# Kernel optimization log

Hardware: AMD Instinct MI355X
Metric: run time of the kernel (lower is better)

The kernel has to match this reference:

```python
import jax, jax.numpy as jnp
import numpy as np

EMBED_DIM = 512
NUM_HEADS = 8
GLOBAL_MIX = 0.5


def setup_inputs() -> dict:
    key = jax.random.key(0)
    ks = jax.random.split(key, 7)
    B, L, E = 8, 1024, EMBED_DIM
    s = 1.0 / np.sqrt(E)
    x = jax.random.normal(ks[0], (B, L, E), dtype=jnp.float32)
    mask = jax.random.randint(ks[1], (B, L), 0, 2) > 0  # True = valid token
    Wq = jax.random.normal(ks[2], (E, E), dtype=jnp.float32) * s
    Wk = jax.random.normal(ks[3], (E, E), dtype=jnp.float32) * s
    Wv = jax.random.normal(ks[4], (E, E), dtype=jnp.float32) * s
    Wo = jax.random.normal(ks[5], (E, E), dtype=jnp.float32) * s
    G = jax.random.normal(ks[6], (L, L), dtype=jnp.float32)
    return {"x": x, "mask": mask, "Wq": Wq, "Wk": Wk, "Wv": Wv, "Wo": Wo, "G": G}


def _tanh_mha(x, mask, Wq, Wk, Wv, Wo, G):
    B, L, E = x.shape
    H = NUM_HEADS
    D = E // H
    scale = 1.0 / np.sqrt(D)
    dt = x.dtype
    fmax = jnp.finfo(dt).max
    tiny = jnp.finfo(dt).tiny

    def split_heads(t):  # (B,L,E) -> (B,H,L,D)
        return t.reshape(B, L, H, D).transpose(0, 2, 1, 3)

    q = split_heads(x @ Wq.T)
    k = split_heads(x @ Wk.T)
    v = split_heads(x @ Wv.T)

    scores = jnp.tanh(jnp.einsum('bhqd,bhkd->bhqk', q, k) * scale)
    key_valid = mask[:, None, None, :]  # (B,1,1,L)
    scores = jnp.where(key_valid, scores, -jnp.inf)

    finite = jnp.isfinite(scores)
    finite_scores = jnp.where(finite, scores, -fmax)
    m = jnp.max(finite_scores, axis=(1, 2, 3), keepdims=True)  # per-sample amax over heads+q+k
    m = jnp.where(jnp.isfinite(m), m, jnp.zeros_like(m))
    exp_scores = jnp.where(finite, jnp.exp(scores - m), jnp.zeros_like(scores))

    mf = mask.astype(dt)
    exp_scores = exp_scores * mf[:, None, None, :] * mf[:, None, :, None]
    denom = jnp.maximum(exp_scores.sum(axis=(1, 2, 3), keepdims=True), tiny)
    weights = exp_scores / denom
    # dropout p=0 -> identity; renorm pass kept for faithfulness
    renorm = jnp.maximum(weights.sum(axis=(1, 2, 3), keepdims=True), tiny)
    weights = weights / renorm

    # learnable global attention: softmax rows, clamp, mask, normalize over (q,k)
    activated = jnp.maximum(jax.nn.softmax(G, axis=-1), 0.0)  # (L,L)
    gscores = activated[None] * mf[:, None, :] * mf[:, :, None]  # (B,L,L)
    gsums = jnp.maximum(gscores.sum(axis=(1, 2), keepdims=True), tiny)
    gnorm = (gscores / gsums)[:, None]  # (B,1,L,L)
    weights = (1.0 - GLOBAL_MIX) * weights + GLOBAL_MIX * gnorm

    attended = jnp.einsum('bhqk,bhkd->bhqd', weights, v)
    attended = attended * mf[:, None, :, None]
    attended = attended.transpose(0, 2, 1, 3).reshape(B, L, E)
    return attended @ Wo.T


def reference(x, mask, Wq, Wk, Wv, Wo, G):
    return _tanh_mha(x, mask, Wq, Wk, Wv, Wo, G)
```

## Files before the change

### kernel.cpp

```cpp
#include <hip/hip_runtime.h>
#include <math.h>

#define B_ 8
#define L_ 1024
#define E_ 512
#define H_ 8
#define D_ 64
#define QSZ (B_*H_*L_*D_)
#define BLE ((size_t)B_*L_*E_)
#define TINYF 1.175494350822287508e-38f
#define SWK(r) ((((r) ^ ((r) >> 3))) & 7)

typedef unsigned short u16;
typedef __attribute__((ext_vector_type(8))) short bfrag;
typedef __attribute__((ext_vector_type(4))) float ffrag;
typedef __attribute__((ext_vector_type(16))) float ffrag16;
typedef __attribute__((ext_vector_type(4))) short vshort4;

#if __has_builtin(__builtin_amdgcn_exp2f)
#define EXP2F(x) __builtin_amdgcn_exp2f(x)
#else
#define EXP2F(x) __expf((x) * 0.6931471805599453f)
#endif
#if __has_builtin(__builtin_amdgcn_rcpf)
#define RCPF(x) __builtin_amdgcn_rcpf(x)
#else
#define RCPF(x) (1.0f / (x))
#endif

__device__ __forceinline__ u16 f2b(float f) {
  unsigned u = __float_as_uint(f);
  u += 0x7fffu + ((u >> 16) & 1u);
  return (u16)(u >> 16);
}
__device__ __forceinline__ unsigned pk2(float a, float b) {
  unsigned ua = __float_as_uint(a); ua += 0x7fffu + ((ua >> 16) & 1u);
  unsigned ub = __float_as_uint(b); ub += 0x7fffu + ((ub >> 16) & 1u);
  return (ua >> 16) | (ub & 0xffff0000u);
}
__device__ __forceinline__ float blo(unsigned u) { return __uint_as_float(u << 16); }
__device__ __forceinline__ float bhi(unsigned u) { return __uint_as_float(u & 0xffff0000u); }

__device__ __forceinline__ bfrag cvt8v(const float* __restrict__ src) {
  float4 a = *(const float4*)src;
  float4 b = *(const float4*)(src + 4);
  bfrag r;
  r[0]=(short)f2b(a.x); r[1]=(short)f2b(a.y); r[2]=(short)f2b(a.z); r[3]=(short)f2b(a.w);
  r[4]=(short)f2b(b.x); r[5]=(short)f2b(b.y); r[6]=(short)f2b(b.z); r[7]=(short)f2b(b.w);
  return r;
}

__device__ __forceinline__ void gll16(const void* g, void* l) {
  __builtin_amdgcn_global_load_lds(
      (const __attribute__((address_space(1))) void*)g,
      (__attribute__((address_space(3))) void*)l, 16, 0, 0);
}

__global__ __launch_bounds__(256) void prep_softmax_k(
    const float* __restrict__ x, const float* __restrict__ Wq,
    const float* __restrict__ Wk, const float* __restrict__ Wv,
    const float* __restrict__ Wo, const float* __restrict__ G,
    const int* __restrict__ mask,
    u16* __restrict__ xb, u16* __restrict__ Wb, u16* __restrict__ actb,
    float* __restrict__ R) {
  const int bid = blockIdx.x, t = threadIdx.x;
  __shared__ float sred[8];
  __shared__ float rred[4][8];
  if (bid < 2048) {
    size_t c = (size_t)bid * 256 + t;
    *(bfrag*)&xb[c * 8] = cvt8v(x + c * 8);
    return;
  }
  if (bid < 2560) {
    const int c2 = bid - 2048;
    const float* src = (c2 < 128) ? Wq : (c2 < 256) ? Wk : (c2 < 384) ? Wv : Wo;
    const size_t base = (size_t)(c2 >> 7) * 262144;
    const size_t cc = (size_t)(c2 & 127) * 256 + t;
    *(bfrag*)&Wb[base + cc * 8] = cvt8v(src + cc * 8);
    return;
  }
  const int q = bid - 2560;
  const int w = t >> 6, lane = t & 63;
  float4 g4 = ((const float4*)(G + (size_t)q * 1024))[t];
  float m = fmaxf(fmaxf(g4.x, g4.y), fmaxf(g4.z, g4.w));
#pragma unroll
  for (int off = 32; off > 0; off >>= 1) m = fmaxf(m, __shfl_down(m, off));
  if (lane == 0) sred[w] = m;
  __syncthreads();
  m = fmaxf(fmaxf(sred[0], sred[1]), fmaxf(sred[2], sred[3]));
  float e0 = __expf(g4.x - m), e1 = __expf(g4.y - m);
  float e2 = __expf(g4.z - m), e3 = __expf(g4.w - m);
  float s = e0 + e1 + e2 + e3;
#pragma unroll
  for (int off = 32; off > 0; off >>= 1) s += __shfl_down(s, off);
  if (lane == 0) sred[4 + w] = s;
  __syncthreads();
  const float inv = 1.0f / (sred[4] + sred[5] + sred[6] + sred[7]);
  const unsigned p0 = pk2(e0 * inv, e1 * inv);
  const unsigned p1 = pk2(e2 * inv, e3 * inv);
  *(uint2*)&actb[(size_t)q * 1024 + t * 4] = make_uint2(p0, p1);
  const float r0 = blo(p0), r1 = bhi(p0);
  const float r2 = blo(p1), r3 = bhi(p1);
  float rd[8];
#pragma unroll
  for (int b = 0; b < 8; ++b) {
    const int* mkp = mask + b * 1024 + t * 4;
    rd[b] = (mkp[0] ? r0 : 0.f) + (mkp[1] ? r1 : 0.f) +
            (mkp[2] ? r2 : 0.f) + (mkp[3] ? r3 : 0.f);
#pragma unroll
    for (int off = 32; off > 0; off >>= 1) rd[b] += __shfl_down(rd[b], off);
  }
  if (lane == 0)
#pragma unroll
    for (int b = 0; b < 8; ++b) rred[w][b] = rd[b];
  __syncthreads();
  if (t < 8) R[q * 8 + t] = rred[0][t] + rred[1][t] + rred[2][t] + rred[3][t];
}

__global__ __launch_bounds__(256) void proj_k(
    const u16* __restrict__ xb, const u16* __restrict__ Wb,
    const int* __restrict__ mask, const float* __restrict__ R,
    float* __restrict__ sums,
    u16* __restrict__ Qb, u16* __restrict__ Kb, u16* __restrict__ Vtb) {
  const int m0 = blockIdx.x * 128;
  const int n0 = blockIdx.y * 128;
  __shared__ __align__(16) u16 As[128 * 64];
  __shared__ __align__(16) u16 Bs[128 * 64];
  __shared__ float rr[4][8];
  const int t = threadIdx.x, w = t >> 6, lane = t & 63;
  const int l15 = lane & 15, quad = lane >> 4;
  const int mq = (w >> 1) * 64, nq = (w & 1) * 64;

  if (blockIdx.x == 0 && blockIdx.y == 0) {
    float a8[8] = {0,0,0,0,0,0,0,0};
    for (int q = t; q < 1024; q += 256)
#pragma unroll
      for (int b = 0; b < 8; ++b)
        if (mask[b * 1024 + q]) a8[b] += R[q * 8 + b];
#pragma unroll
    for (int b = 0; b < 8; ++b) {
#pragma unroll
      for (int off = 32; off > 0; off >>= 1) a8[b] += __shfl_down(a8[b], off);
    }
    if (lane == 0)
#pragma unroll
      for (int b = 0; b < 8; ++b) rr[w][b] = a8[b];
    __syncthreads();
    if (t < 8) {
      sums[t] = 0.0f;
      sums[8 + t] = rr[0][t] + rr[1][t] + rr[2][t] + rr[3][t];
    }
  }

  const ffrag fz = {0.f, 0.f, 0.f, 0.f};
  ffrag acc[4][4];
#pragma unroll
  for (int i = 0; i < 4; ++i)
#pragma unroll
    for (int j = 0; j < 4; ++j) acc[i][j] = fz;

  for (int kk = 0; kk < 512; kk += 64) {
    __syncthreads();
#pragma unroll
    for (int j = 0; j < 4; ++j) {
      const int c = w * 256 + j * 64 + lane;
      const int row = c >> 3, ck = (c & 7) ^ (row & 7);
      gll16(xb + (size_t)(m0 + row) * 512 + kk + ck * 8,
            &As[(size_t)(w * 256 + j * 64) * 8]);
    }
#pragma unroll
    for (int j = 0; j < 4; ++j) {
      const int c = w * 256 + j * 64 + lane;
      const int row = c >> 3, ck = (c & 7) ^ (row & 7);
      gll16(Wb + (size_t)(n0 + row) * 512 + kk + ck * 8,
            &Bs[(size_t)(w * 256 + j * 64) * 8]);
    }
    __syncthreads();
#pragma unroll
    for (int s = 0; s < 2; ++s) {
      bfrag av[4], bv[4];
#pragma unroll
      for (int i = 0; i < 4; ++i) {
        const int ar = mq + i * 16 + l15;
        av[i] = *(const bfrag*)&As[ar * 64 + (((quad + 4 * s) ^ (ar & 7)) << 3)];
        const int br = nq + i * 16 + l15;
        bv[i] = *(const bfrag*)&Bs[br * 64 + (((quad + 4 * s) ^ (br & 7)) << 3)];
      }
#pragma unroll
      for (int i = 0; i < 4; ++i)
#pragma unroll
        for (int j = 0; j < 4; ++j)
          acc[i][j] = __builtin_amdgcn_mfma_f32_16x16x32_bf16(av[i], bv[j], acc[i][j], 0, 0, 0);
    }
  }
  const int z = n0 >> 9;
  const int c0 = n0 & 511;
#pragma unroll
  for (int i = 0; i < 4; ++i) {
    const int mbase = m0 + mq + i * 16 + quad * 4;
    const int b = mbase >> 10, l0 = mbase & 1023;
#pragma unroll
    for (int j = 0; j < 4; ++j) {
      const int nc = c0 + nq + j * 16 + l15;
      const int h = nc >> 6, d = nc & 63;
      if (z == 0) {
        u16* dst = Qb + ((size_t)(b * 8 + h) * 1024 + l0) * 64 + d;
#pragma unroll
        for (int r = 0; r < 4; ++r) dst[(size_t)r * 64] = f2b(acc[i][j][r]);
      } else if (z == 1) {
        u16* dst = Kb + ((size_t)(b * 8 + h) * 1024 + l0) * 64 + d;
#pragma unroll
        for (int r = 0; r < 4; ++r) dst[(size_t)r * 64] = f2b(acc[i][j][r]);
      } else {
        vshort4 vs;
#pragma unroll
        for (int r = 0; r < 4; ++r)
          vs[r] = (short)(mask[b * 1024 + l0 + r] ? f2b(acc[i][j][r]) : (u16)0);
        *(vshort4*)(Vtb + ((size_t)(b * 8 + h) * 64 + d) * 1024 + l0) = vs;
      }
    }
  }
}

__global__ __launch_bounds__(256) void attn_gv_k(
    const u16* __restrict__ Qb, const u16* __restrict__ Kb,
    const u16* __restrict__ Vtb, const u16* __restrict__ actb,
    const int* __restrict__ mask,
    u16* __restrict__ AEb, u16* __restrict__ AGb, float* __restrict__ denom) {
  __shared__ __align__(16) u16 POOL[13320];
  const int t = threadIdx.x, w = t >> 6, lane = t & 63;
  const int l15 = lane & 15, quad = lane >> 4;

  if (blockIdx.x < 512) {
    u16* As = POOL;
    u16* Bs = POOL + 4096;
    const int mt = blockIdx.x & 127, nt = blockIdx.x >> 7;
    const int m0 = mt * 64, n0 = nt * 128;
    const int b = mt >> 4;
    const int q0 = (mt & 15) * 64;
    const int mq = (w >> 1) * 32, nq = (w & 1) * 64;
    const ffrag fz = {0.f, 0.f, 0.f, 0.f};
    ffrag acc[2][4];
#pragma unroll
    for (int i = 0; i < 2; ++i)
#pragma unroll
      for (int j = 0; j < 4; ++j) acc[i][j] = fz;

    for (int kk = 0; kk < 1024; kk += 64) {
      __syncthreads();
#pragma unroll
      for (int j = 0; j < 2; ++j) {
        const int c = w * 128 + j * 64 + lane;
        const int row = c >> 3, ck = (c & 7) ^ (row & 7);
        gll16(actb + (size_t)(q0 + row) * 1024 + kk + ck * 8,
              &As[(size_t)(w * 128 + j * 64) * 8]);
      }
#pragma unroll
      for (int j = 0; j < 4; ++j) {
        const int c = w * 256 + j * 64 + lane;
        const int row = c >> 3, ck = (c & 7) ^ (row & 7);
        gll16(Vtb + (size_t)(b * 512 + n0 + row) * 1024 + kk + ck * 8,
              &Bs[(size_t)(w * 256 + j * 64) * 8]);
      }
      __syncthreads();
#pragma unroll
      for (int s = 0; s < 2; ++s) {
        bfrag av[2], bv[4];
#pragma unroll
        for (int i = 0; i < 2; ++i) {
          const int ar = mq + i * 16 + l15;
          av[i] = *(const bfrag*)&As[ar * 64 + (((quad + 4 * s) ^ (ar & 7)) << 3)];
        }
#pragma unroll
        for (int j = 0; j < 4; ++j) {
          const int br = nq + j * 16 + l15;
          bv[j] = *(const bfrag*)&Bs[br * 64 + (((quad + 4 * s) ^ (br & 7)) << 3)];
        }
#pragma unroll
        for (int i = 0; i < 2; ++i)
#pragma unroll
          for (int j = 0; j < 4; ++j)
            acc[i][j] = __builtin_amdgcn_mfma_f32_16x16x32_bf16(av[i], bv[j], acc[i][j], 0, 0, 0);
      }
    }
#pragma unroll
    for (int i = 0; i < 2; ++i) {
      const int mbase = m0 + mq + i * 16 + quad * 4;
#pragma unroll
      for (int j = 0; j < 4; ++j) {
        const int n = n0 + nq + j * 16 + l15;
#pragma unroll
        for (int r = 0; r < 4; ++r)
          AGb[(size_t)(mbase + r) * 512 + n] = f2b(acc[i][j][r]);
      }
    }
    return;
  }

  const int aid = blockIdx.x - 512;
  const int qt = aid & 15;
  const int bh = aid >> 4;
  const int b = bh >> 3, h = bh & 7;
  u16* Ks = POOL;
  u16* Vs = POOL + 4096;
  u16* Es = POOL + 8192;
  u16* Ms = POOL + 12288;
  float* red4 = (float*)(POOL + 13312);
  const int l31 = lane & 31, hi = lane >> 5;
  const int qsb = w >> 1, msb = w & 1;
  const int qpb = w & 1, dpb = w >> 1;

  const u16* Kg = Kb + (size_t)bh * 65536;
  const u16* Vg = Vtb + (size_t)bh * 65536;

  const u16* Qrow = Qb + ((size_t)bh * 1024 + qt * 64 + qsb * 32 + l31) * 64;
  bfrag qf[4];
#pragma unroll
  for (int ko = 0; ko < 4; ++ko) qf[ko] = *(const bfrag*)(Qrow + ko * 16 + hi * 8);

  {
    int4 mi = *(const int4*)(mask + b * 1024 + t * 4);
    vshort4 mv;
    mv[0] = mi.x ? (short)0x3F80 : (short)0; mv[1] = mi.y ? (short)0x3F80 : (short)0;
    mv[2] = mi.z ? (short)0x3F80 : (short)0; mv[3] = mi.w ? (short)0x3F80 : (short)0;
    *(vshort4*)&Ms[t * 4] = mv;
  }

  auto stageK = [&](int kt) {
#pragma unroll
    for (int j = 0; j < 2; ++j) {
      const int c = w * 128 + j * 64 + lane;
      const int row = c >> 3, ck = (c & 7) ^ SWK(row);
      gll16(Kg + (size_t)(kt * 64 + row) * 64 + ck * 8,
            &Ks[(size_t)(w * 128 + j * 64) * 8]);
    }
  };
  auto stageV = [&](int kt) {
#pragma unroll
    for (int j = 0; j < 2; ++j) {
      const int c = w * 128 + j * 64 + lane;
      const int row = c >> 3, ck = (c & 7) ^ SWK(row);
      gll16(Vg + (size_t)row * 1024 + kt * 64 + ck * 8,
            &Vs[(size_t)(w * 128 + j * 64) * 8]);
    }
  };

  stageK(0); stageV(0);
  __syncthreads();

  ffrag16 accE, dacc;
#pragma unroll
  for (int i = 0; i < 16; ++i) { accE[i] = 0.f; dacc[i] = 0.f; }

  for (int kt = 0; kt < 16; ++kt) {
    ffrag16 st;
#pragma unroll
    for (int i = 0; i < 16; ++i) st[i] = 0.f;
    const int krow = msb * 32 + l31;
    const int kk7 = SWK(krow);
#pragma unroll
    for (int ko = 0; ko < 4; ++ko) {
      bfrag ak = *(const bfrag*)&Ks[krow * 64 + (((ko * 2 + hi) ^ kk7) << 3)];
      st = __builtin_amdgcn_mfma_f32_32x32x16_bf16(ak, qf[ko], st, 0, 0, 0);
    }
    const int qrow = qsb * 32 + l31;
    const int qk7 = SWK(qrow);
#pragma unroll
    for (int g = 0; g < 4; ++g) {
      float ee[4];
#pragma unroll
      for (int r = 0; r < 4; ++r) {
        const float tt = EXP2F(st[4 * g + r] * 0.360673760222f);
        ee[r] = EXP2F(RCPF(tt + 1.0f) * -2.88539008178f);
      }
      const int k0 = msb * 32 + g * 8 + hi * 4;
      *(uint2*)&Es[qrow * 64 + (((k0 >> 3) ^ qk7) << 3) + (k0 & 7)] =
          make_uint2(pk2(ee[0], ee[1]), pk2(ee[2], ee[3]));
    }
    __syncthreads();
    if (kt < 15) stageK(kt + 1);

    const int erow = qpb * 32 + l31;
    const int ek7 = SWK(erow);
    const int vrow = dpb * 32 + l31;
    const int vk7 = SWK(vrow);
#pragma unroll
    for (int ko = 0; ko < 4; ++ko) {
      const int co = ko * 2 + hi;
      bfrag ea = *(const bfrag*)&Es[erow * 64 + ((co ^ ek7) << 3)];
      bfrag bv = *(const bfrag*)&Vs[vrow * 64 + ((co ^ vk7) << 3)];
      accE = __builtin_amdgcn_mfma_f32_32x32x16_bf16(ea, bv, accE, 0, 0, 0);
      if (dpb == 0) {
        bfrag bm = *(const bfrag*)&Ms[kt * 64 + ko * 16 + hi * 8];
        dacc = __builtin_amdgcn_mfma_f32_32x32x16_bf16(ea, bm, dacc, 0, 0, 0);
      }
    }
    __syncthreads();
    if (kt < 15) stageV(kt + 1);
  }

  const size_t obase = ((size_t)(b * 1024 + qt * 64 + qpb * 32)) * 512
                       + h * 64 + dpb * 32 + l31;
#pragma unroll
  for (int r = 0; r < 16; ++r) {
    const int qloc = (r & 3) + 8 * (r >> 2) + 4 * hi;
    AEb[obase + (size_t)qloc * 512] = f2b(accE[r]);
  }
  float dsumv = 0.0f;
  if (l31 == 0 && dpb == 0) {
    const int qb0 = b * 1024 + qt * 64 + qpb * 32 + 4 * hi;
#pragma unroll
    for (int r = 0; r < 16; ++r) {
      const int q = qb0 + (r & 3) + 8 * (r >> 2);
      dsumv += mask[q] ? dacc[r] : 0.0f;
    }
    red4[qpb * 2 + hi] = dsumv;
  }
  __syncthreads();
  if (t == 0) atomicAdd(denom + b, red4[0] + red4[1] + red4[2] + red4[3]);
}

__global__ __launch_bounds__(256) void o_proj_k(
    const u16* __restrict__ AEb, const u16* __restrict__ AGb,
    const int* __restrict__ mask, const float* __restrict__ sums,
    const u16* __restrict__ Wb, float* __restrict__ out) {
  const int m0 = blockIdx.x * 128;
  const int n0 = blockIdx.y * 128;
  const int b = m0 >> 10;
  const float c1 = 0.5f / fmaxf(sums[b], TINYF);
  const float c2 = 0.5f / fmaxf(sums[8 + b], TINYF);
  __shared__ __align__(16) u16 As[128 * 64];
  __shared__ __align__(16) u16 Bs[128 * 64];
  const int t = threadIdx.x, w = t >> 6, lane = t & 63;
  const int l15 = lane & 15, quad = lane >> 4;
  const int mq = (w >> 1) * 64, nq = (w & 1) * 64;
  int rowi[4]; float c1r[4], c2r[4];
#pragma unroll
  for (int i = 0; i < 4; ++i) {
    const int c = t + i * 256;
    rowi[i] = c >> 3;
    const int mqv = mask[b * 1024 + ((m0 + rowi[i]) & 1023)];
    c1r[i] = mqv ? c1 : 0.0f;
    c2r[i] = mqv ? c2 : 0.0f;
  }
  const ffrag fz = {0.f, 0.f, 0.f, 0.f};
  ffrag acc[4][4];
#pragma unroll
  for (int i = 0; i < 4; ++i)
#pragma unroll
    for (int j = 0; j < 4; ++j) acc[i][j] = fz;

  for (int kk = 0; kk < 512; kk += 64) {
    __syncthreads();
#pragma unroll
    for (int i = 0; i < 4; ++i) {
      const int c = t + i * 256;
      const int row = rowi[i], ck = c & 7;
      const size_t gofs = (size_t)(m0 + row) * 512 + kk + ck * 8;
      uint4 ua = *(const uint4*)(AEb + gofs);
      uint4 ug = *(const uint4*)(AGb + gofs);
      const float a1 = c1r[i], a2 = c2r[i];
      uint4 res;
      res.x = pk2(a1 * blo(ua.x) + a2 * blo(ug.x), a1 * bhi(ua.x) + a2 * bhi(ug.x));
      res.y = pk2(a1 * blo(ua.y) + a2 * blo(ug.y), a1 * bhi(ua.y) + a2 * bhi(ug.y));
      res.z = pk2(a1 * blo(ua.z) + a2 * blo(ug.z), a1 * bhi(ua.z) + a2 * bhi(ug.z));
      res.w = pk2(a1 * blo(ua.w) + a2 * blo(ug.w), a1 * bhi(ua.w) + a2 * bhi(ug.w));
      *(uint4*)&As[row * 64 + ((ck ^ (row & 7)) << 3)] = res;
    }
#pragma unroll
    for (int j = 0; j < 4; ++j) {
      const int c = w * 256 + j * 64 + lane;
      const int row = c >> 3, ck = (c & 7) ^ (row & 7);
      gll16(Wb + (size_t)(1536 + n0 + row) * 512 + kk + ck * 8,
            &Bs[(size_t)(w * 256 + j * 64) * 8]);
    }
    __syncthreads();
#pragma unroll
    for (int s = 0; s < 2; ++s) {
      bfrag av[4], bv[4];
#pragma unroll
      for (int i = 0; i < 4; ++i) {
        const int ar = mq + i * 16 + l15;
        av[i] = *(const bfrag*)&As[ar * 64 + (((quad + 4 * s) ^ (ar & 7)) << 3)];
        const int br = nq + i * 16 + l15;
        bv[i] = *(const bfrag*)&Bs[br * 64 + (((quad + 4 * s) ^ (br & 7)) << 3)];
      }
#pragma unroll
      for (int i = 0; i < 4; ++i)
#pragma unroll
        for (int j = 0; j < 4; ++j)
          acc[i][j] = __builtin_amdgcn_mfma_f32_16x16x32_bf16(av[i], bv[j], acc[i][j], 0, 0, 0);
    }
  }
#pragma unroll
  for (int i = 0; i < 4; ++i) {
    const int mbase = m0 + mq + i * 16 + quad * 4;
#pragma unroll
    for (int j = 0; j < 4; ++j) {
      const int n = n0 + nq + j * 16 + l15;
#pragma unroll
      for (int r = 0; r < 4; ++r)
        out[(size_t)(mbase + r) * 512 + n] = acc[i][j][r];
    }
  }
}

extern "C" void kernel_launch(void* const* d_in, const int* in_sizes, int n_in,
                              void* d_out, int out_size, void* d_ws, size_t ws_size,
                              hipStream_t stream) {
  const float* x  = (const float*)d_in[0];
  const int* mask = (const int*)d_in[1];
  const float* Wq = (const float*)d_in[2];
  const float* Wk = (const float*)d_in[3];
  const float* Wv = (const float*)d_in[4];
  const float* Wo = (const float*)d_in[5];
  const float* G  = (const float*)d_in[6];
  float* out = (float*)d_out;

  u16* xb   = (u16*)d_ws;
  u16* Wb   = xb + (size_t)8192 * 512;
  u16* Qb   = Wb + (size_t)2048 * 512;
  u16* Kb   = Qb + QSZ;
  u16* Vtb  = Kb + QSZ;
  u16* actb = Vtb + QSZ;
  u16* AEb  = actb + (size_t)1024 * 1024;
  u16* AGb  = AEb + BLE;
  float* R  = (float*)(AGb + BLE);
  float* SUMS = R + 8192;

  prep_softmax_k<<<3584, 256, 0, stream>>>(x, Wq, Wk, Wv, Wo, G, mask, xb, Wb, actb, R);
  proj_k<<<dim3(64, 12), 256, 0, stream>>>(xb, Wb, mask, R, SUMS, Qb, Kb, Vtb);
  attn_gv_k<<<1536, 256, 0, stream>>>(Qb, Kb, Vtb, actb, mask, AEb, AGb, SUMS);
  o_proj_k<<<dim3(64, 4), 256, 0, stream>>>(AEb, AGb, mask, SUMS, Wb, out);
}
```

Measured before the change: 183.8 us.

## Keep P in registers, double-buffer K/V, enlarge global-attention GEMM tiles

The attention branch now builds the exp-score MFMA operand directly in registers through lane shuffles, instead of writing it to shared memory and reading it back. K and V tiles are double-buffered so the next tile loads while the current one computes, which removes one barrier per iteration. Each wave now covers all 64 output columns over half the key range, and the two halves are reduced through shared memory at the end. The global-attention GEMM blocks grow from 64x128 to 128x128 tiles, which halves that block count and raises per-block reuse. The cost is more registers and LDS per block, which may lower occupancy.

```diff
diff --git a/kernel.cpp b/kernel.cpp
--- a/kernel.cpp
+++ b/kernel.cpp
@@ -16,6 +16,7 @@
 typedef __attribute__((ext_vector_type(4))) float ffrag;
 typedef __attribute__((ext_vector_type(16))) float ffrag16;
 typedef __attribute__((ext_vector_type(4))) short vshort4;
+typedef __attribute__((ext_vector_type(4))) unsigned ufrag;
 
 #if __has_builtin(__builtin_amdgcn_exp2f)
 #define EXP2F(x) __builtin_amdgcn_exp2f(x)
@@ -227,33 +228,33 @@
     const u16* __restrict__ Vtb, const u16* __restrict__ actb,
     const int* __restrict__ mask,
     u16* __restrict__ AEb, u16* __restrict__ AGb, float* __restrict__ denom) {
-  __shared__ __align__(16) u16 POOL[13320];
+  __shared__ __align__(16) u16 POOL[17424];
   const int t = threadIdx.x, w = t >> 6, lane = t & 63;
   const int l15 = lane & 15, quad = lane >> 4;
 
-  if (blockIdx.x < 512) {
+  if (blockIdx.x < 256) {
     u16* As = POOL;
-    u16* Bs = POOL + 4096;
-    const int mt = blockIdx.x & 127, nt = blockIdx.x >> 7;
-    const int m0 = mt * 64, n0 = nt * 128;
-    const int b = mt >> 4;
-    const int q0 = (mt & 15) * 64;
-    const int mq = (w >> 1) * 32, nq = (w & 1) * 64;
+    u16* Bs = POOL + 8192;
+    const int b = blockIdx.x >> 5;
+    const int mt = (blockIdx.x >> 2) & 7;
+    const int nt = blockIdx.x & 3;
+    const int m0 = mt * 128, n0 = nt * 128;
+    const int mq = (w >> 1) * 64, nq = (w & 1) * 64;
     const ffrag fz = {0.f, 0.f, 0.f, 0.f};
-    ffrag acc[2][4];
-#pragma unroll
-    for (int i = 0; i < 2; ++i)
+    ffrag acc[4][4];
+#pragma unroll
+    for (int i = 0; i < 4; ++i)
 #pragma unroll
       for (int j = 0; j < 4; ++j) acc[i][j] = fz;
 
     for (int kk = 0; kk < 1024; kk += 64) {
       __syncthreads();
 #pragma unroll
-      for (int j = 0; j < 2; ++j) {
-        const int c = w * 128 + j * 64 + lane;
+      for (int j = 0; j < 4; ++j) {
+        const int c = w * 256 + j * 64 + lane;
         const int row = c >> 3, ck = (c & 7) ^ (row & 7);
-        gll16(actb + (size_t)(q0 + row) * 1024 + kk + ck * 8,
-              &As[(size_t)(w * 128 + j * 64) * 8]);
+        gll16(actb + (size_t)(m0 + row) * 1024 + kk + ck * 8,
+              &As[(size_t)(w * 256 + j * 64) * 8]);
       }
 #pragma unroll
       for (int j = 0; j < 4; ++j) {
@@ -265,50 +266,43 @@
       __syncthreads();
 #pragma unroll
       for (int s = 0; s < 2; ++s) {
-        bfrag av[2], bv[4];
-#pragma unroll
-        for (int i = 0; i < 2; ++i) {
+        bfrag av[4], bv[4];
+#pragma unroll
+        for (int i = 0; i < 4; ++i) {
           const int ar = mq + i * 16 + l15;
           av[i] = *(const bfrag*)&As[ar * 64 + (((quad + 4 * s) ^ (ar & 7)) << 3)];
+          const int br = nq + i * 16 + l15;
+          bv[i] = *(const bfrag*)&Bs[br * 64 + (((quad + 4 * s) ^ (br & 7)) << 3)];
         }
 #pragma unroll
-        for (int j = 0; j < 4; ++j) {
-          const int br = nq + j * 16 + l15;
-          bv[j] = *(const bfrag*)&Bs[br * 64 + (((quad + 4 * s) ^ (br & 7)) << 3)];
-        }
-#pragma unroll
-        for (int i = 0; i < 2; ++i)
+        for (int i = 0; i < 4; ++i)
 #pragma unroll
           for (int j = 0; j < 4; ++j)
             acc[i][j] = __builtin_amdgcn_mfma_f32_16x16x32_bf16(av[i], bv[j], acc[i][j], 0, 0, 0);
       }
     }
 #pragma unroll
-    for (int i = 0; i < 2; ++i) {
+    for (int i = 0; i < 4; ++i) {
       const int mbase = m0 + mq + i * 16 + quad * 4;
 #pragma unroll
       for (int j = 0; j < 4; ++j) {
         const int n = n0 + nq + j * 16 + l15;
 #pragma unroll
         for (int r = 0; r < 4; ++r)
-          AGb[(size_t)(mbase + r) * 512 + n] = f2b(acc[i][j][r]);
+          AGb[(size_t)(b * 1024 + mbase + r) * 512 + n] = f2b(acc[i][j][r]);
       }
     }
     return;
   }
 
-  const int aid = blockIdx.x - 512;
+  const int aid = blockIdx.x - 256;
   const int qt = aid & 15;
   const int bh = aid >> 4;
   const int b = bh >> 3, h = bh & 7;
-  u16* Ks = POOL;
-  u16* Vs = POOL + 4096;
-  u16* Es = POOL + 8192;
-  u16* Ms = POOL + 12288;
-  float* red4 = (float*)(POOL + 13312);
+  u16* Ms = POOL + 16384;
+  float* red8 = (float*)(POOL + 17408);
   const int l31 = lane & 31, hi = lane >> 5;
   const int qsb = w >> 1, msb = w & 1;
-  const int qpb = w & 1, dpb = w >> 1;
 
   const u16* Kg = Kb + (size_t)bh * 65536;
   const u16* Vg = Vtb + (size_t)bh * 65536;
@@ -326,45 +320,54 @@
     *(vshort4*)&Ms[t * 4] = mv;
   }
 
-  auto stageK = [&](int kt) {
+  auto stageK = [&](int kt, u16* dst) {
 #pragma unroll
     for (int j = 0; j < 2; ++j) {
       const int c = w * 128 + j * 64 + lane;
       const int row = c >> 3, ck = (c & 7) ^ SWK(row);
       gll16(Kg + (size_t)(kt * 64 + row) * 64 + ck * 8,
-            &Ks[(size_t)(w * 128 + j * 64) * 8]);
+            &dst[(size_t)(w * 128 + j * 64) * 8]);
     }
   };
-  auto stageV = [&](int kt) {
+  auto stageV = [&](int kt, u16* dst) {
 #pragma unroll
     for (int j = 0; j < 2; ++j) {
       const int c = w * 128 + j * 64 + lane;
       const int row = c >> 3, ck = (c & 7) ^ SWK(row);
       gll16(Vg + (size_t)row * 1024 + kt * 64 + ck * 8,
-            &Vs[(size_t)(w * 128 + j * 64) * 8]);
+            &dst[(size_t)(w * 128 + j * 64) * 8]);
     }
   };
 
-  stageK(0); stageV(0);
+  stageK(0, POOL); stageV(0, POOL + 8192);
   __syncthreads();
 
-  ffrag16 accE, dacc;
-#pragma unroll
-  for (int i = 0; i < 16; ++i) { accE[i] = 0.f; dacc[i] = 0.f; }
+  ffrag16 accE0, accE1, dacc;
+#pragma unroll
+  for (int i = 0; i < 16; ++i) { accE0[i] = 0.f; accE1[i] = 0.f; dacc[i] = 0.f; }
+
+  const int krow = msb * 32 + l31;
+  const int kk7 = SWK(krow);
+  const int vr0 = l31, vr1 = 32 + l31;
+  const int vk70 = SWK(vr0), vk71 = SWK(vr1);
 
   for (int kt = 0; kt < 16; ++kt) {
+    const int cur = kt & 1;
+    u16* Kc = POOL + (cur << 12);
+    u16* Vc = POOL + 8192 + (cur << 12);
+    if (kt < 15) {
+      stageK(kt + 1, POOL + ((cur ^ 1) << 12));
+      stageV(kt + 1, POOL + 8192 + ((cur ^ 1) << 12));
+    }
     ffrag16 st;
 #pragma unroll
     for (int i = 0; i < 16; ++i) st[i] = 0.f;
-    const int krow = msb * 32 + l31;
-    const int kk7 = SWK(krow);
 #pragma unroll
     for (int ko = 0; ko < 4; ++ko) {
-      bfrag ak = *(const bfrag*)&Ks[krow * 64 + (((ko * 2 + hi) ^ kk7) << 3)];
+      bfrag ak = *(const bfrag*)&Kc[krow * 64 + (((ko * 2 + hi) ^ kk7) << 3)];
       st = __builtin_amdgcn_mfma_f32_32x32x16_bf16(ak, qf[ko], st, 0, 0, 0);
     }
-    const int qrow = qsb * 32 + l31;
-    const int qk7 = SWK(qrow);
+    unsigned P[4][2];
 #pragma unroll
     for (int g = 0; g < 4; ++g) {
       float ee[4];
@@ -373,51 +376,67 @@
         const float tt = EXP2F(st[4 * g + r] * 0.360673760222f);
         ee[r] = EXP2F(RCPF(tt + 1.0f) * -2.88539008178f);
       }
-      const int k0 = msb * 32 + g * 8 + hi * 4;
-      *(uint2*)&Es[qrow * 64 + (((k0 >> 3) ^ qk7) << 3) + (k0 & 7)] =
-          make_uint2(pk2(ee[0], ee[1]), pk2(ee[2], ee[3]));
+      P[g][0] = pk2(ee[0], ee[1]);
+      P[g][1] = pk2(ee[2], ee[3]);
+    }
+#pragma unroll
+    for (int kc = 0; kc < 2; ++kc) {
+      const unsigned a0 = P[2 * kc][0],     a1 = P[2 * kc][1];
+      const unsigned b0 = P[2 * kc + 1][0], b1 = P[2 * kc + 1][1];
+      const unsigned xa0 = (unsigned)__shfl_xor((int)a0, 32);
+      const unsigned xa1 = (unsigned)__shfl_xor((int)a1, 32);
+      const unsigned xb0 = (unsigned)__shfl_xor((int)b0, 32);
+      const unsigned xb1 = (unsigned)__shfl_xor((int)b1, 32);
+      ufrag au;
+      au[0] = hi ? xb0 : a0;  au[1] = hi ? xb1 : a1;
+      au[2] = hi ? b0 : xa0;  au[3] = hi ? b1 : xa1;
+      const bfrag af = __builtin_bit_cast(bfrag, au);
+      const int kchunk = msb * 4 + kc * 2 + hi;
+      bfrag bv0 = *(const bfrag*)&Vc[vr0 * 64 + ((kchunk ^ vk70) << 3)];
+      bfrag bv1 = *(const bfrag*)&Vc[vr1 * 64 + ((kchunk ^ vk71) << 3)];
+      accE0 = __builtin_amdgcn_mfma_f32_32x32x16_bf16(af, bv0, accE0, 0, 0, 0);
+      accE1 = __builtin_amdgcn_mfma_f32_32x32x16_bf16(af, bv1, accE1, 0, 0, 0);
+      bfrag bm = *(const bfrag*)&Ms[kt * 64 + msb * 32 + kc * 16 + hi * 8];
+      dacc = __builtin_amdgcn_mfma_f32_32x32x16_bf16(af, bm, dacc, 0, 0, 0);
     }
     __syncthreads();
-    if (kt < 15) stageK(kt + 1);
-
-    const int erow = qpb * 32 + l31;
-    const int ek7 = SWK(erow);
-    const int vrow = dpb * 32 + l31;
-    const int vk7 = SWK(vrow);
-#pragma unroll
-    for (int ko = 0; ko < 4; ++ko) {
-      const int co = ko * 2 + hi;
-      bfrag ea = *(const bfrag*)&Es[erow * 64 + ((co ^ ek7) << 3)];
-      bfrag bv = *(const bfrag*)&Vs[vrow * 64 + ((co ^ vk7) << 3)];
-      accE = __builtin_amdgcn_mfma_f32_32x32x16_bf16(ea, bv, accE, 0, 0, 0);
-      if (dpb == 0) {
-        bfrag bm = *(const bfrag*)&Ms[kt * 64 + ko * 16 + hi * 8];
-        dacc = __builtin_amdgcn_mfma_f32_32x32x16_bf16(ea, bm, dacc, 0, 0, 0);
-      }
-    }
-    __syncthreads();
-    if (kt < 15) stageV(kt + 1);
-  }
-
-  const size_t obase = ((size_t)(b * 1024 + qt * 64 + qpb * 32)) * 512
-                       + h * 64 + dpb * 32 + l31;
-#pragma unroll
-  for (int r = 0; r < 16; ++r) {
-    const int qloc = (r & 3) + 8 * (r >> 2) + 4 * hi;
-    AEb[obase + (size_t)qloc * 512] = f2b(accE[r]);
-  }
-  float dsumv = 0.0f;
-  if (l31 == 0 && dpb == 0) {
-    const int qb0 = b * 1024 + qt * 64 + qpb * 32 + 4 * hi;
+  }
+
+  if (l31 == 0) {
+    float dsumv = 0.0f;
+    const int qb0 = b * 1024 + qt * 64 + qsb * 32 + 4 * hi;
 #pragma unroll
     for (int r = 0; r < 16; ++r) {
       const int q = qb0 + (r & 3) + 8 * (r >> 2);
       dsumv += mask[q] ? dacc[r] : 0.0f;
     }
-    red4[qpb * 2 + hi] = dsumv;
+    red8[w * 2 + hi] = dsumv;
+  }
+  float* Ered = (float*)POOL;
+  if (msb == 1) {
+#pragma unroll
+    for (int r = 0; r < 16; ++r) {
+      const int qloc = (r & 3) + 8 * (r >> 2) + 4 * hi;
+      Ered[(qsb * 32 + qloc) * 64 + l31] = accE0[r];
+      Ered[(qsb * 32 + qloc) * 64 + 32 + l31] = accE1[r];
+    }
   }
   __syncthreads();
-  if (t == 0) atomicAdd(denom + b, red4[0] + red4[1] + red4[2] + red4[3]);
+  if (msb == 0) {
+    const size_t obase = ((size_t)(b * 1024 + qt * 64 + qsb * 32)) * 512
+                         + h * 64 + l31;
+#pragma unroll
+    for (int r = 0; r < 16; ++r) {
+      const int qloc = (r & 3) + 8 * (r >> 2) + 4 * hi;
+      const float v0 = accE0[r] + Ered[(qsb * 32 + qloc) * 64 + l31];
+      const float v1 = accE1[r] + Ered[(qsb * 32 + qloc) * 64 + 32 + l31];
+      AEb[obase + (size_t)qloc * 512] = f2b(v0);
+      AEb[obase + (size_t)qloc * 512 + 32] = f2b(v1);
+    }
+  }
+  if (t == 0)
+    atomicAdd(denom + b, red8[0] + red8[1] + red8[2] + red8[3] +
+                         red8[4] + red8[5] + red8[6] + red8[7]);
 }
 
 __global__ __launch_bounds__(256) void o_proj_k(
@@ -530,6 +549,6 @@
 
   prep_softmax_k<<<3584, 256, 0, stream>>>(x, Wq, Wk, Wv, Wo, G, mask, xb, Wb, actb, R);
   proj_k<<<dim3(64, 12), 256, 0, stream>>>(xb, Wb, mask, R, SUMS, Qb, Kb, Vtb);
-  attn_gv_k<<<1536, 256, 0, stream>>>(Qb, Kb, Vtb, actb, mask, AEb, AGb, SUMS);
+  attn_gv_k<<<1280, 256, 0, stream>>>(Qb, Kb, Vtb, actb, mask, AEb, AGb, SUMS);
   o_proj_k<<<dim3(64, 4), 256, 0, stream>>>(AEb, AGb, mask, SUMS, Wb, out);
 }
```

Measured after the change: 193.8 us. 1.05x slower.

## Split attention key range across two blocks and sum partials in output projection

Applied to the files above, without the earlier changes.

Each attention block now processes half of the key tiles (8 instead of 16), doubling the attention grid from 1024 to 2048 blocks. The two partial E·V results go to separate bf16 buffers (the second reuses the xb workspace), and the output projection loads both and adds them before scaling. The aim is more parallelism and shorter per-block loops. The cost is an extra bf16 round-trip of the attention output, an extra load in o_proj, one more atomic per block on the denominator, and partials rounded to bf16 before they are summed.

```diff
diff --git a/kernel.cpp b/kernel.cpp
--- a/kernel.cpp
+++ b/kernel.cpp
@@ -226,7 +226,8 @@
     const u16* __restrict__ Qb, const u16* __restrict__ Kb,
     const u16* __restrict__ Vtb, const u16* __restrict__ actb,
     const int* __restrict__ mask,
-    u16* __restrict__ AEb, u16* __restrict__ AGb, float* __restrict__ denom) {
+    u16* __restrict__ AEb, u16* __restrict__ AE1b, u16* __restrict__ AGb,
+    float* __restrict__ denom) {
   __shared__ __align__(16) u16 POOL[13320];
   const int t = threadIdx.x, w = t >> 6, lane = t & 63;
   const int l15 = lane & 15, quad = lane >> 4;
@@ -298,9 +299,11 @@
   }
 
   const int aid = blockIdx.x - 512;
-  const int qt = aid & 15;
-  const int bh = aid >> 4;
+  const int kh = aid & 1;
+  const int qt = (aid >> 1) & 15;
+  const int bh = aid >> 5;
   const int b = bh >> 3, h = bh & 7;
+  const int kt0 = kh * 8;
   u16* Ks = POOL;
   u16* Vs = POOL + 4096;
   u16* Es = POOL + 8192;
@@ -345,14 +348,14 @@
     }
   };
 
-  stageK(0); stageV(0);
+  stageK(kt0); stageV(kt0);
   __syncthreads();
 
   ffrag16 accE, dacc;
 #pragma unroll
   for (int i = 0; i < 16; ++i) { accE[i] = 0.f; dacc[i] = 0.f; }
 
-  for (int kt = 0; kt < 16; ++kt) {
+  for (int kt = kt0; kt < kt0 + 8; ++kt) {
     ffrag16 st;
 #pragma unroll
     for (int i = 0; i < 16; ++i) st[i] = 0.f;
@@ -378,7 +381,7 @@
           make_uint2(pk2(ee[0], ee[1]), pk2(ee[2], ee[3]));
     }
     __syncthreads();
-    if (kt < 15) stageK(kt + 1);
+    if (kt < kt0 + 7) stageK(kt + 1);
 
     const int erow = qpb * 32 + l31;
     const int ek7 = SWK(erow);
@@ -396,15 +399,16 @@
       }
     }
     __syncthreads();
-    if (kt < 15) stageV(kt + 1);
-  }
-
+    if (kt < kt0 + 7) stageV(kt + 1);
+  }
+
+  u16* AEo = kh ? AE1b : AEb;
   const size_t obase = ((size_t)(b * 1024 + qt * 64 + qpb * 32)) * 512
                        + h * 64 + dpb * 32 + l31;
 #pragma unroll
   for (int r = 0; r < 16; ++r) {
     const int qloc = (r & 3) + 8 * (r >> 2) + 4 * hi;
-    AEb[obase + (size_t)qloc * 512] = f2b(accE[r]);
+    AEo[obase + (size_t)qloc * 512] = f2b(accE[r]);
   }
   float dsumv = 0.0f;
   if (l31 == 0 && dpb == 0) {
@@ -421,7 +425,8 @@
 }
 
 __global__ __launch_bounds__(256) void o_proj_k(
-    const u16* __restrict__ AEb, const u16* __restrict__ AGb,
+    const u16* __restrict__ AEb, const u16* __restrict__ AE1b,
+    const u16* __restrict__ AGb,
     const int* __restrict__ mask, const float* __restrict__ sums,
     const u16* __restrict__ Wb, float* __restrict__ out) {
   const int m0 = blockIdx.x * 128;
@@ -458,13 +463,18 @@
       const int row = rowi[i], ck = c & 7;
       const size_t gofs = (size_t)(m0 + row) * 512 + kk + ck * 8;
       uint4 ua = *(const uint4*)(AEb + gofs);
+      uint4 ub = *(const uint4*)(AE1b + gofs);
       uint4 ug = *(const uint4*)(AGb + gofs);
       const float a1 = c1r[i], a2 = c2r[i];
       uint4 res;
-      res.x = pk2(a1 * blo(ua.x) + a2 * blo(ug.x), a1 * bhi(ua.x) + a2 * bhi(ug.x));
-      res.y = pk2(a1 * blo(ua.y) + a2 * blo(ug.y), a1 * bhi(ua.y) + a2 * bhi(ug.y));
-      res.z = pk2(a1 * blo(ua.z) + a2 * blo(ug.z), a1 * bhi(ua.z) + a2 * bhi(ug.z));
-      res.w = pk2(a1 * blo(ua.w) + a2 * blo(ug.w), a1 * bhi(ua.w) + a2 * bhi(ug.w));
+      res.x = pk2(a1 * (blo(ua.x) + blo(ub.x)) + a2 * blo(ug.x),
+                  a1 * (bhi(ua.x) + bhi(ub.x)) + a2 * bhi(ug.x));
+      res.y = pk2(a1 * (blo(ua.y) + blo(ub.y)) + a2 * blo(ug.y),
+                  a1 * (bhi(ua.y) + bhi(ub.y)) + a2 * bhi(ug.y));
+      res.z = pk2(a1 * (blo(ua.z) + blo(ub.z)) + a2 * blo(ug.z),
+                  a1 * (bhi(ua.z) + bhi(ub.z)) + a2 * bhi(ug.z));
+      res.w = pk2(a1 * (blo(ua.w) + blo(ub.w)) + a2 * blo(ug.w),
+                  a1 * (bhi(ua.w) + bhi(ub.w)) + a2 * bhi(ug.w));
       *(uint4*)&As[row * 64 + ((ck ^ (row & 7)) << 3)] = res;
     }
 #pragma unroll
@@ -527,9 +537,10 @@
   u16* AGb  = AEb + BLE;
   float* R  = (float*)(AGb + BLE);
   float* SUMS = R + 8192;
+  u16* AE1b = xb;
 
   prep_softmax_k<<<3584, 256, 0, stream>>>(x, Wq, Wk, Wv, Wo, G, mask, xb, Wb, actb, R);
   proj_k<<<dim3(64, 12), 256, 0, stream>>>(xb, Wb, mask, R, SUMS, Qb, Kb, Vtb);
-  attn_gv_k<<<1536, 256, 0, stream>>>(Qb, Kb, Vtb, actb, mask, AEb, AGb, SUMS);
-  o_proj_k<<<dim3(64, 4), 256, 0, stream>>>(AEb, AGb, mask, SUMS, Wb, out);
-}
+  attn_gv_k<<<2560, 256, 0, stream>>>(Qb, Kb, Vtb, actb, mask, AEb, AE1b, AGb, SUMS);
+  o_proj_k<<<dim3(64, 4), 256, 0, stream>>>(AEb, AE1b, AGb, mask, SUMS, Wb, out);
+}
```

Result: slower. 191.3 us (+4.1%).

## Load K/V MFMA fragments directly into registers with double-buffered prefetch

Applied to the files above, without the earlier changes.

The attention branch no longer stages K and V tiles through LDS. Each lane loads its MFMA operand fragments straight from global memory into registers, ping-ponging two register sets so the next tile is prefetched while the current one computes. Shared memory shrinks, and the barriers become raw s_barrier calls with manual lgkmcnt waits. This removes LDS staging traffic and some synchronization, at the cost of more VGPRs and uncoalesced per-lane global reads, since K and V are loaded redundantly by the wave pairs that share them.

```diff
diff --git a/kernel.cpp b/kernel.cpp
--- a/kernel.cpp
+++ b/kernel.cpp
@@ -227,7 +227,7 @@
     const u16* __restrict__ Vtb, const u16* __restrict__ actb,
     const int* __restrict__ mask,
     u16* __restrict__ AEb, u16* __restrict__ AGb, float* __restrict__ denom) {
-  __shared__ __align__(16) u16 POOL[13320];
+  __shared__ __align__(16) u16 POOL[12292];
   const int t = threadIdx.x, w = t >> 6, lane = t & 63;
   const int l15 = lane & 15, quad = lane >> 4;
 
@@ -301,11 +301,9 @@
   const int qt = aid & 15;
   const int bh = aid >> 4;
   const int b = bh >> 3, h = bh & 7;
-  u16* Ks = POOL;
-  u16* Vs = POOL + 4096;
-  u16* Es = POOL + 8192;
-  u16* Ms = POOL + 12288;
-  float* red4 = (float*)(POOL + 13312);
+  u16* Es = POOL;
+  u16* Ms = POOL + 4096;
+  float* red4 = (float*)(POOL + 5120);
   const int l31 = lane & 31, hi = lane >> 5;
   const int qsb = w >> 1, msb = w & 1;
   const int qpb = w & 1, dpb = w >> 1;
@@ -326,45 +324,40 @@
     *(vshort4*)&Ms[t * 4] = mv;
   }
 
-  auto stageK = [&](int kt) {
-#pragma unroll
-    for (int j = 0; j < 2; ++j) {
-      const int c = w * 128 + j * 64 + lane;
-      const int row = c >> 3, ck = (c & 7) ^ SWK(row);
-      gll16(Kg + (size_t)(kt * 64 + row) * 64 + ck * 8,
-            &Ks[(size_t)(w * 128 + j * 64) * 8]);
-    }
-  };
-  auto stageV = [&](int kt) {
-#pragma unroll
-    for (int j = 0; j < 2; ++j) {
-      const int c = w * 128 + j * 64 + lane;
-      const int row = c >> 3, ck = (c & 7) ^ SWK(row);
-      gll16(Vg + (size_t)row * 1024 + kt * 64 + ck * 8,
-            &Vs[(size_t)(w * 128 + j * 64) * 8]);
-    }
-  };
-
-  stageK(0); stageV(0);
+  const int krow = msb * 32 + l31;
+  const int vrow = dpb * 32 + l31;
+  const int qrow = qsb * 32 + l31;
+  const int qk7 = SWK(qrow);
+  const int erow = qpb * 32 + l31;
+  const int ek7 = SWK(erow);
+
+  ffrag16 accE, dacc;
+#pragma unroll
+  for (int i = 0; i < 16; ++i) { accE[i] = 0.f; dacc[i] = 0.f; }
+
+  bfrag ka[4], va[4], kb_[4], vb_[4];
+#pragma unroll
+  for (int ko = 0; ko < 4; ++ko) {
+    ka[ko] = *(const bfrag*)(Kg + (size_t)krow * 64 + (ko * 2 + hi) * 8);
+    va[ko] = *(const bfrag*)(Vg + (size_t)vrow * 1024 + (ko * 2 + hi) * 8);
+  }
   __syncthreads();
 
-  ffrag16 accE, dacc;
-#pragma unroll
-  for (int i = 0; i < 16; ++i) { accE[i] = 0.f; dacc[i] = 0.f; }
-
-  for (int kt = 0; kt < 16; ++kt) {
+  auto step = [&](int kt, bfrag (&kc)[4], bfrag (&vc)[4],
+                  bfrag (&kn)[4], bfrag (&vn)[4], bool pf) {
+    if (pf) {
+#pragma unroll
+      for (int ko = 0; ko < 4; ++ko) {
+        kn[ko] = *(const bfrag*)(Kg + (size_t)((kt + 1) * 64 + krow) * 64 + (ko * 2 + hi) * 8);
+        vn[ko] = *(const bfrag*)(Vg + (size_t)vrow * 1024 + (kt + 1) * 64 + (ko * 2 + hi) * 8);
+      }
+    }
     ffrag16 st;
 #pragma unroll
     for (int i = 0; i < 16; ++i) st[i] = 0.f;
-    const int krow = msb * 32 + l31;
-    const int kk7 = SWK(krow);
-#pragma unroll
-    for (int ko = 0; ko < 4; ++ko) {
-      bfrag ak = *(const bfrag*)&Ks[krow * 64 + (((ko * 2 + hi) ^ kk7) << 3)];
-      st = __builtin_amdgcn_mfma_f32_32x32x16_bf16(ak, qf[ko], st, 0, 0, 0);
-    }
-    const int qrow = qsb * 32 + l31;
-    const int qk7 = SWK(qrow);
+#pragma unroll
+    for (int ko = 0; ko < 4; ++ko)
+      st = __builtin_amdgcn_mfma_f32_32x32x16_bf16(kc[ko], qf[ko], st, 0, 0, 0);
 #pragma unroll
     for (int g = 0; g < 4; ++g) {
       float ee[4];
@@ -377,26 +370,27 @@
       *(uint2*)&Es[qrow * 64 + (((k0 >> 3) ^ qk7) << 3) + (k0 & 7)] =
           make_uint2(pk2(ee[0], ee[1]), pk2(ee[2], ee[3]));
     }
-    __syncthreads();
-    if (kt < 15) stageK(kt + 1);
-
-    const int erow = qpb * 32 + l31;
-    const int ek7 = SWK(erow);
-    const int vrow = dpb * 32 + l31;
-    const int vk7 = SWK(vrow);
+    asm volatile("s_waitcnt lgkmcnt(0)" ::: "memory");
+    __builtin_amdgcn_s_barrier();
+    asm volatile("" ::: "memory");
 #pragma unroll
     for (int ko = 0; ko < 4; ++ko) {
       const int co = ko * 2 + hi;
       bfrag ea = *(const bfrag*)&Es[erow * 64 + ((co ^ ek7) << 3)];
-      bfrag bv = *(const bfrag*)&Vs[vrow * 64 + ((co ^ vk7) << 3)];
-      accE = __builtin_amdgcn_mfma_f32_32x32x16_bf16(ea, bv, accE, 0, 0, 0);
+      accE = __builtin_amdgcn_mfma_f32_32x32x16_bf16(ea, vc[ko], accE, 0, 0, 0);
       if (dpb == 0) {
         bfrag bm = *(const bfrag*)&Ms[kt * 64 + ko * 16 + hi * 8];
         dacc = __builtin_amdgcn_mfma_f32_32x32x16_bf16(ea, bm, dacc, 0, 0, 0);
       }
     }
-    __syncthreads();
-    if (kt < 15) stageV(kt + 1);
+    asm volatile("" ::: "memory");
+    __builtin_amdgcn_s_barrier();
+    asm volatile("" ::: "memory");
+  };
+
+  for (int kt2 = 0; kt2 < 16; kt2 += 2) {
+    step(kt2, ka, va, kb_, vb_, true);
+    step(kt2 + 1, kb_, vb_, ka, va, kt2 < 14);
   }
 
   const size_t obase = ((size_t)(b * 1024 + qt * 64 + qpb * 32)) * 512
```

Result: slower. 215.5 us (+17.3%).
